# Kernel tuning notes

Hardware: AMD Instinct MI355X
Metric: run time of the kernel (lower is better)

The kernel has to match this reference:

```python
import jax, jax.numpy as jnp
import numpy as np
from jax import lax

THRESH = 0.6      # pnet score threshold (threshold[0])
IOU_THR = 0.5     # per-scale nms threshold in detect_face
K_PICKS = 128     # fixed max number of NMS picks (jit-static)
STRIDE = 2.0
CELL = 12.0
NEG = -1e30


def _conv(x, w, b):
    y = lax.conv_general_dilated(x, w, (1, 1), 'VALID',
                                 dimension_numbers=('NCHW', 'OIHW', 'NCHW'))
    return y + b[None, :, None, None]


def _prelu(x, a):
    return jnp.where(x > 0, x, a[None, :, None, None] * x)


def _maxpool2(x):
    return lax.reduce_window(x, -jnp.inf, lax.max, (1, 1, 2, 2), (1, 1, 2, 2), 'VALID')


def _nms(boxes, scores):
    # Greedy union-IoU NMS (nms_numpy math), vectorized with a fixed pick budget.
    # boxes [N,4] (shared grid), scores [N] with invalid entries already = NEG.
    x1, y1, x2, y2 = boxes[:, 0], boxes[:, 1], boxes[:, 2], boxes[:, 3]
    area = (x2 - x1 + 1.0) * (y2 - y1 + 1.0)

    def body(live, _):
        j = jnp.argmax(live)
        s = live[j]
        ok = s > NEG * 0.5
        xx1 = jnp.maximum(x1[j], x1); yy1 = jnp.maximum(y1[j], y1)
        xx2 = jnp.minimum(x2[j], x2); yy2 = jnp.minimum(y2[j], y2)
        inter = jnp.maximum(0.0, xx2 - xx1 + 1.0) * jnp.maximum(0.0, yy2 - yy1 + 1.0)
        iou = inter / (area[j] + area - inter)
        live = jnp.where(iou > IOU_THR, NEG, live).at[j].set(NEG)
        return live, (j, ok)

    _, (idx, ok) = lax.scan(body, scores, None, length=K_PICKS)
    return idx, ok


def setup_inputs():
    key = jax.random.key(0)
    ks = jax.random.split(key, 16)
    B, H, W = 16, 384, 512
    f = lambda k, shp, s=0.1: jax.random.normal(k, shp, jnp.float32) * s
    return {
        'im_data': jax.random.uniform(ks[0], (B, 3, H, W), jnp.float32) * 255.0,
        'c1_w': f(ks[1], (10, 3, 3, 3)), 'c1_b': f(ks[2], (10,)),
        'p1': jnp.full((10,), 0.25, jnp.float32),
        'c2_w': f(ks[3], (16, 10, 3, 3)), 'c2_b': f(ks[4], (16,)),
        'p2': jnp.full((16,), 0.25, jnp.float32),
        'c3_w': f(ks[5], (32, 16, 3, 3)), 'c3_b': f(ks[6], (32,)),
        'p3': jnp.full((32,), 0.25, jnp.float32),
        'c41_w': f(ks[7], (2, 32, 1, 1)), 'c41_b': f(ks[8], (2,)),
        'c42_w': f(ks[9], (4, 32, 1, 1)), 'c42_b': f(ks[10], (4,)),
    }


def reference(im_data, c1_w, c1_b, p1, c2_w, c2_b, p2, c3_w, c3_b, p3,
              c41_w, c41_b, c42_w, c42_b):
    # --- PNet conv trunk (detect_face normalization + MTCNN PNet) ---
    x = (im_data - 127.5) * 0.0078125
    h = _prelu(_conv(x, c1_w, c1_b), p1)
    h = _maxpool2(h)                                   # 2x2 s2 (dims even -> ceil==floor)
    h = _prelu(_conv(h, c2_w, c2_b), p2)
    h = _prelu(_conv(h, c3_w, c3_b), p3)
    probs = jax.nn.softmax(_conv(h, c41_w, c41_b), axis=1)[:, 1]   # [B,Hp,Wp]
    reg = _conv(h, c42_w, c42_b)                                   # [B,4,Hp,Wp]

    # --- generateBoundingBox (dense, masked instead of nonzero; scale=1) ---
    B, Hp, Wp = probs.shape
    yy, xx = jnp.meshgrid(jnp.arange(Hp, dtype=jnp.float32),
                          jnp.arange(Wp, dtype=jnp.float32), indexing='ij')
    boxes4 = jnp.stack([jnp.floor(STRIDE * xx + 1.0).ravel(),
                        jnp.floor(STRIDE * yy + 1.0).ravel(),
                        jnp.floor(STRIDE * xx + CELL).ravel(),
                        jnp.floor(STRIDE * yy + CELL).ravel()], axis=1)  # [N,4]
    scores = probs.reshape(B, -1)                                   # [B,N]
    regf = reg.reshape(B, 4, -1).transpose(0, 2, 1)                 # [B,N,4]
    masked = jnp.where(scores >= THRESH, scores, NEG)

    # --- per-image greedy NMS (batched_nms: images independent) ---
    idx, ok = jax.vmap(_nms, in_axes=(None, 0))(boxes4, masked)     # [B,K]
    pb = boxes4[idx]                                                # [B,K,4]
    ps = jnp.take_along_axis(scores, idx, axis=1)                   # [B,K]
    pr = jnp.take_along_axis(regf, idx[..., None], axis=1)          # [B,K,4]

    w = pb[..., 2] - pb[..., 0]
    hh = pb[..., 3] - pb[..., 1]
    q1 = pb[..., 0] + pr[..., 0] * w
    q2 = pb[..., 1] + pr[..., 1] * hh
    q3 = pb[..., 2] + pr[..., 2] * w
    q4 = pb[..., 3] + pr[..., 3] * hh
    rw = q3 - q1
    rh = q4 - q2
    l = jnp.maximum(rw, rh)
    nx1 = q1 + rw * 0.5 - l * 0.5
    ny1 = q2 + rh * 0.5 - l * 0.5
    out = jnp.stack([nx1, ny1, nx1 + l, ny1 + l, ps], axis=-1)      # [B,K,5]
    return out * ok[..., None].astype(out.dtype)
```

## Files before the change

kernel.cpp:

```cpp
#include <hip/hip_runtime.h>
#include <math.h>

#define BATCH 16
#define IH 384
#define IW 512
#define C1 10
#define P1H 191
#define P1W 255
#define P1S 256
#define C2 16
#define H2 189
#define W2 253
#define C3 32
#define H3 187
#define W3 251
#define N3 (H3*W3)
#define KP 128
#define CAP 7680
#define NEGV (-1e30f)

typedef _Float16 f16x8 __attribute__((ext_vector_type(8)));
typedef _Float16 f16x4 __attribute__((ext_vector_type(4)));
typedef float    f32x16 __attribute__((ext_vector_type(16)));

#define PXT 66
#define PXT2 68
#define NSUB 2

#define T1R 34
#define T1C 68
__global__ __launch_bounds__(256, 1) void k_conv1pool(
        const float* __restrict__ im, const float* __restrict__ w,
        const float* __restrict__ bia, const float* __restrict__ slope,
        float* __restrict__ outp,
        const float* __restrict__ w3, const float* __restrict__ w2,
        _Float16* __restrict__ wbuf, _Float16* __restrict__ wbuf2) {
    __shared__ float T[3 * T1R * T1C];

    int tx = threadIdx.x, ty = threadIdx.y;
    int tid = ty * 16 + tx;
    int bx = blockIdx.x, by = blockIdx.y, bb = blockIdx.z;

    if (bx == 0 && by == 0 && bb == 0) {
        for (int e = tid; e < 4608; e += 256) {
            int oc = e / 144;
            int rem = e - oc * 144;
            int ic = rem / 9;
            int tap = rem - ic * 9;
            float v = w3[e];
            _Float16 h = (_Float16)v;
            _Float16 l = (_Float16)(v - (float)h);
            int d = ((tap * 2 + (ic >> 3)) * 32 + oc) * 8 + (ic & 7);
            wbuf[d] = h;
            wbuf[4608 + d] = l;
        }
        for (int e = tid; e < 4608; e += 256) {
            int tap = e / 512;
            int rem = e - tap * 512;
            int half = rem >> 8;
            int oc = (rem >> 3) & 31;
            int j = e & 7;
            int ic = half * 8 + j;
            float v = 0.f;
            if (oc < 16 && ic < 10) v = w2[(oc * 10 + ic) * 9 + tap];
            _Float16 h = (_Float16)v;
            wbuf2[e] = h;
            wbuf2[4608 + e] = (_Float16)(v - (float)h);
        }
    }

    const size_t ibase = (size_t)bb * 3 * IH * IW;
    for (int g = tid; g < 3 * T1R * 33; g += 256) {
        int ch = g / (T1R * 33);
        int rem = g - ch * (T1R * 33);
        int r = rem / 33;
        int c2 = rem - r * 33;
        int yg = 32 * by + r;
        int xg = 64 * bx + 2 * c2;
        float2 v = make_float2(0.f, 0.f);
        if (yg < IH && xg < IW)
            v = *(const float2*)(im + ibase + ((size_t)ch * IH + yg) * IW + xg);
        float2 o;
        o.x = (v.x - 127.5f) * 0.0078125f;
        o.y = (v.y - 127.5f) * 0.0078125f;
        *(float2*)&T[(ch * T1R + r) * T1C + 2 * c2] = o;
    }
    __syncthreads();

    int Y  = by * 16 + ty;
    int X0 = bx * 32 + 2 * tx;
    if (Y >= P1H) return;

    float win[3][4][6];
    #pragma unroll
    for (int ch = 0; ch < 3; ++ch)
        #pragma unroll
        for (int r = 0; r < 4; ++r) {
            const float* p = &T[(ch * T1R + 2 * ty + r) * T1C + 4 * tx];
            float4 a = *(const float4*)p;
            float2 b = *(const float2*)(p + 4);
            win[ch][r][0] = a.x; win[ch][r][1] = a.y;
            win[ch][r][2] = a.z; win[ch][r][3] = a.w;
            win[ch][r][4] = b.x; win[ch][r][5] = b.y;
        }
    #pragma unroll
    for (int ch = 0; ch < 3; ++ch)
        #pragma unroll
        for (int r = 0; r < 4; ++r)
            #pragma unroll
            for (int c = 0; c < 6; ++c)
                asm volatile("" : "+v"(win[ch][r][c]));

    bool px1ok = (X0 + 1 < P1W);
    for (int oc = 0; oc < C1; ++oc) {
        const float* wo = w + oc * 27;
        float bv = bia[oc], sv = slope[oc];
        float c0 = bv, c1 = bv, c2 = bv, c3 = bv;
        float c4 = bv, c5 = bv, c6 = bv, c7 = bv;
        #pragma unroll
        for (int ch = 0; ch < 3; ++ch)
            #pragma unroll
            for (int ky = 0; ky < 3; ++ky)
                #pragma unroll
                for (int kx = 0; kx < 3; ++kx) {
                    float wv = wo[(ch * 3 + ky) * 3 + kx];
                    c0 += win[ch][0 + ky][0 + kx] * wv;
                    c1 += win[ch][0 + ky][1 + kx] * wv;
                    c2 += win[ch][0 + ky][2 + kx] * wv;
                    c3 += win[ch][0 + ky][3 + kx] * wv;
                    c4 += win[ch][1 + ky][0 + kx] * wv;
                    c5 += win[ch][1 + ky][1 + kx] * wv;
                    c6 += win[ch][1 + ky][2 + kx] * wv;
                    c7 += win[ch][1 + ky][3 + kx] * wv;
                }
        float m0 = fmaxf(fmaxf(c0, c1), fmaxf(c4, c5));
        float m1 = fmaxf(fmaxf(c2, c3), fmaxf(c6, c7));
        float p0 = m0 > 0.f ? m0 : sv * m0;
        float p1 = m1 > 0.f ? m1 : sv * m1;
        float* o = outp + (((size_t)bb * C1 + oc) * P1H + Y) * P1S + X0;
        if (px1ok) *(float2*)o = make_float2(p0, p1);
        else       o[0] = p0;
    }
}

__global__ __launch_bounds__(256, 2) void k_conv2mfma(
        const float* __restrict__ pool1,
        const _Float16* __restrict__ wbuf2,
        const float* __restrict__ b2, const float* __restrict__ s2,
        float* __restrict__ outp) {
    __shared__ __align__(16) _Float16 Ah[6 * 2 * PXT2 * 8];
    __shared__ __align__(16) _Float16 Al[6 * 2 * PXT2 * 8];
    __shared__ float htab[32];

    int tid = threadIdx.x;
    int bx = blockIdx.x * 64;
    int by = blockIdx.y * 4;
    int bb = blockIdx.z;

    if (tid < 32) htab[tid] = (tid < 16) ? b2[tid] : s2[tid - 16];

    {
        const float* pin = pool1 + (size_t)bb * C1 * P1H * P1S;
        for (int e = tid; e < 6 * 16 * 17; e += 256) {
            int row = e / (16 * 17);
            int rem = e - row * (16 * 17);
            int ic  = rem / 17;
            int c4  = (rem - ic * 17) * 4;
            int yg = by + row;
            int xg = bx + c4;
            float4 v = make_float4(0.f, 0.f, 0.f, 0.f);
            if (ic < C1 && yg < P1H) {
                const float* src = pin + ((size_t)ic * P1H + yg) * P1S + xg;
                if (xg + 3 < P1W) v = *(const float4*)src;
                else {
                    if (xg     < P1W) v.x = src[0];
                    if (xg + 1 < P1W) v.y = src[1];
                    if (xg + 2 < P1W) v.z = src[2];
                }
            }
            int kg = ic >> 3, j = ic & 7;
            int base = ((row * 2 + kg) * PXT2 + c4) * 8 + j;
            _Float16 h;
            h = (_Float16)v.x; Ah[base]      = h; Al[base]      = (_Float16)(v.x - (float)h);
            h = (_Float16)v.y; Ah[base + 8]  = h; Al[base + 8]  = (_Float16)(v.y - (float)h);
            h = (_Float16)v.z; Ah[base + 16] = h; Al[base + 16] = (_Float16)(v.z - (float)h);
            h = (_Float16)v.w; Ah[base + 24] = h; Al[base + 24] = (_Float16)(v.w - (float)h);
        }
    }
    __syncthreads();

    int wv = tid >> 6, lane = tid & 63;
    int col = lane & 31, half = lane >> 5;
    int y = by + wv;
    if (y >= H2) return;

    f32x16 acc[NSUB];
    #pragma unroll
    for (int s = 0; s < NSUB; ++s)
        #pragma unroll
        for (int i = 0; i < 16; ++i) acc[s][i] = 0.f;

    const _Float16* wg = wbuf2 + (half * 32 + col) * 8;

    #pragma unroll 1
    for (int ky = 0; ky < 3; ++ky) {
        const _Float16* arh = Ah + ((wv + ky) * 2 + half) * (PXT2 * 8);
        const _Float16* arl = Al + ((wv + ky) * 2 + half) * (PXT2 * 8);
        #pragma unroll
        for (int kx = 0; kx < 3; ++kx) {
            int tap = ky * 3 + kx;
            f16x8 wh = *(const f16x8*)(wg + tap * 512);
            f16x8 wl = *(const f16x8*)(wg + 4608 + tap * 512);
            #pragma unroll
            for (int s = 0; s < NSUB; ++s) {
                int p = s * 32 + col + kx;
                f16x8 bh = *(const f16x8*)(arh + p * 8);
                f16x8 bl = *(const f16x8*)(arl + p * 8);
                acc[s] = __builtin_amdgcn_mfma_f32_32x32x16_f16(wh, bh, acc[s], 0, 0, 0);
                acc[s] = __builtin_amdgcn_mfma_f32_32x32x16_f16(wl, bh, acc[s], 0, 0, 0);
                acc[s] = __builtin_amdgcn_mfma_f32_32x32x16_f16(wh, bl, acc[s], 0, 0, 0);
            }
        }
    }

    int oc0 = 4 * half, oc1 = 8 + 4 * half;
    #pragma unroll
    for (int s = 0; s < NSUB; ++s) {
        int px = bx + s * 32 + col;
        if (px < W2) {
            float q[8];
            #pragma unroll
            for (int r = 0; r < 8; ++r) {
                int oc = (r < 4) ? (oc0 + r) : (oc1 + r - 4);
                float v = acc[s][r] + htab[oc];
                float sl = htab[16 + oc];
                q[r] = v > 0.f ? v : sl * v;
            }
            float* o = outp + (((size_t)bb * H2 + y) * W2 + px) * C2;
            *(float4*)(o + oc0) = make_float4(q[0], q[1], q[2], q[3]);
            *(float4*)(o + oc1) = make_float4(q[4], q[5], q[6], q[7]);
        }
    }
}

__global__ __launch_bounds__(256, 2) void k_conv3mfma(
        const float* __restrict__ act,
        const _Float16* __restrict__ wbuf,
        const float* __restrict__ b3, const float* __restrict__ s3,
        const float* __restrict__ w41, const float* __restrict__ b41,
        const float* __restrict__ w42, const float* __restrict__ b42,
        float* __restrict__ scores, float4* __restrict__ regf) {
    __shared__ __align__(16) _Float16 Ah[6 * 2 * PXT * 8];
    __shared__ __align__(16) _Float16 Al[6 * 2 * PXT * 8];
    __shared__ __align__(16) float    htab[32 * 8];

    int tid = threadIdx.x;
    int bx = blockIdx.x * (NSUB * 32);
    int by = blockIdx.y * 4;
    int bb = blockIdx.z;

    {
        int oc = tid >> 3, f = tid & 7;
        float v;
        if      (f == 0) v = b3[oc];
        else if (f == 1) v = s3[oc];
        else if (f == 2) v = w41[oc];
        else if (f == 3) v = w41[32 + oc];
        else             v = w42[(f - 4) * 32 + oc];
        htab[tid] = v;
    }
    {
        const float* actb = act + (size_t)bb * H2 * W2 * C2;
        for (int e = tid; e < 6 * PXT * 4; e += 256) {
            int ic4 = e & 3;
            int t = e >> 2;
            int px = t % PXT;
            int row = t / PXT;
            int yg = by + row, xg = bx + px;
            float4 v = make_float4(0.f, 0.f, 0.f, 0.f);
            if (yg < H2 && xg < W2)
                v = *(const float4*)(actb + ((size_t)yg * W2 + xg) * C2 + ic4 * 4);
            float xs0 = v.x, xs1 = v.y, xs2 = v.z, xs3 = v.w;
            f16x4 hv, lv;
            _Float16 h;
            h = (_Float16)xs0; hv[0] = h; lv[0] = (_Float16)(xs0 - (float)h);
            h = (_Float16)xs1; hv[1] = h; lv[1] = (_Float16)(xs1 - (float)h);
            h = (_Float16)xs2; hv[2] = h; lv[2] = (_Float16)(xs2 - (float)h);
            h = (_Float16)xs3; hv[3] = h; lv[3] = (_Float16)(xs3 - (float)h);
            int kg = ic4 >> 1, h4 = ic4 & 1;
            int gr = (row * 2 + kg) * PXT + px;
            *(f16x4*)(Ah + gr * 8 + h4 * 4) = hv;
            *(f16x4*)(Al + gr * 8 + h4 * 4) = lv;
        }
    }
    __syncthreads();

    int wv = tid >> 6, lane = tid & 63;
    int col = lane & 31, half = lane >> 5;
    int y = by + wv;
    if (y >= H3) return;

    f32x16 acc[NSUB];
    #pragma unroll
    for (int s = 0; s < NSUB; ++s)
        #pragma unroll
        for (int i = 0; i < 16; ++i) acc[s][i] = 0.f;

    const _Float16* wg = wbuf + (half * 32 + col) * 8;

    #pragma unroll 1
    for (int ky = 0; ky < 3; ++ky) {
        const _Float16* arh = Ah + ((wv + ky) * 2 + half) * (PXT * 8);
        const _Float16* arl = Al + ((wv + ky) * 2 + half) * (PXT * 8);
        #pragma unroll
        for (int kx = 0; kx < 3; ++kx) {
            int tap = ky * 3 + kx;
            f16x8 wh = *(const f16x8*)(wg + tap * 512);
            f16x8 wl = *(const f16x8*)(wg + 4608 + tap * 512);
            #pragma unroll
            for (int s = 0; s < NSUB; ++s) {
                int p = s * 32 + col + kx;
                f16x8 bh = *(const f16x8*)(arh + p * 8);
                f16x8 bl = *(const f16x8*)(arl + p * 8);
                acc[s] = __builtin_amdgcn_mfma_f32_32x32x16_f16(wh, bh, acc[s], 0, 0, 0);
                acc[s] = __builtin_amdgcn_mfma_f32_32x32x16_f16(wl, bh, acc[s], 0, 0, 0);
                acc[s] = __builtin_amdgcn_mfma_f32_32x32x16_f16(wh, bl, acc[s], 0, 0, 0);
            }
        }
    }

    float L0[NSUB], L1[NSUB], R0[NSUB], R1[NSUB], R2[NSUB], R3[NSUB];
    #pragma unroll
    for (int s = 0; s < NSUB; ++s) { L0[s]=0.f; L1[s]=0.f; R0[s]=0.f; R1[s]=0.f; R2[s]=0.f; R3[s]=0.f; }

    #pragma unroll
    for (int r = 0; r < 16; ++r) {
        int oc = (r & 3) + 8 * (r >> 2) + 4 * half;
        float4 t0 = *(const float4*)&htab[oc * 8];
        float4 t1 = *(const float4*)&htab[oc * 8 + 4];
        #pragma unroll
        for (int s = 0; s < NSUB; ++s) {
            float v = acc[s][r] + t0.x;
            v = v > 0.f ? v : v * t0.y;
            L0[s] += v * t0.z; L1[s] += v * t0.w;
            R0[s] += v * t1.x; R1[s] += v * t1.y;
            R2[s] += v * t1.z; R3[s] += v * t1.w;
        }
    }

    float hb0 = b41[0], hb1 = b41[1];
    float rb0 = b42[0], rb1 = b42[1], rb2 = b42[2], rb3 = b42[3];

    #pragma unroll
    for (int s = 0; s < NSUB; ++s) {
        float l0 = L0[s] + __shfl_xor(L0[s], 32) + hb0;
        float l1 = L1[s] + __shfl_xor(L1[s], 32) + hb1;
        float r0 = R0[s] + __shfl_xor(R0[s], 32) + rb0;
        float r1 = R1[s] + __shfl_xor(R1[s], 32) + rb1;
        float r2 = R2[s] + __shfl_xor(R2[s], 32) + rb2;
        float r3 = R3[s] + __shfl_xor(R3[s], 32) + rb3;
        float m = fmaxf(l0, l1);
        float e0 = expf(l0 - m), e1 = expf(l1 - m);
        float p = e1 / (e0 + e1);
        int px = bx + s * 32 + col;
        if (half == 0 && px < W3) {
            size_t n = (size_t)bb * N3 + (size_t)y * W3 + px;
            scores[n] = (p >= 0.6f) ? p : NEGV;
            regf[n] = make_float4(r0, r1, r2, r3);
        }
    }
}

__global__ __launch_bounds__(512) void k_nms(
        const float* __restrict__ scores, const float4* __restrict__ regf,
        float* __restrict__ outp) {
    __shared__ float s_score[CAP];
    __shared__ int   s_idx[CAP];
    __shared__ float r_s[2][8];
    __shared__ int   r_i[2][8];
    __shared__ float s_picks[KP];
    __shared__ int   s_picki[KP];
    __shared__ int   s_misc[4];

    int tid = threadIdx.x;
    int bb = blockIdx.x;
    const float* sc = scores + (size_t)bb * N3;

    if (tid < 4) s_misc[tid] = 0;
    __syncthreads();

    int cnt = 0;
    for (int i = tid; i < N3; i += 512) if (sc[i] > 0.f) cnt++;
    atomicAdd(&s_misc[0], cnt);
    __syncthreads();
    int M = s_misc[0];

    int cutbin = 0;
    if (M > CAP) {
        for (int i = tid; i < 2048; i += 512) s_idx[i] = 0;
        __syncthreads();
        for (int i = tid; i < N3; i += 512) {
            float s = sc[i];
            if (s > 0.f) {
                int b = (int)((s - 0.6f) * 5120.f);
                b = b < 0 ? 0 : (b > 2047 ? 2047 : b);
                atomicAdd(&s_idx[b], 1);
            }
        }
        __syncthreads();
        if (tid == 0) {
            int accum = 0, b = 2047;
            for (; b >= 0; --b) {
                int c = s_idx[b];
                if (accum + c > CAP) break;
                accum += c;
            }
            s_misc[2] = b + 1;
        }
        __syncthreads();
        cutbin = s_misc[2];
        __syncthreads();
    }

    for (int i = tid; i < N3; i += 512) {
        float s = sc[i];
        if (s > 0.f) {
            bool keep = true;
            if (M > CAP) {
                int b = (int)((s - 0.6f) * 5120.f);
                b = b < 0 ? 0 : (b > 2047 ? 2047 : b);
                keep = (b >= cutbin);
            }
            if (keep) {
                int pos = atomicAdd(&s_misc[1], 1);
                if (pos < CAP) { s_score[pos] = s; s_idx[pos] = i; }
            }
        }
    }
    __syncthreads();
    int M2 = s_misc[1]; if (M2 > CAP) M2 = CAP;

    int np = 0;
    int   ppi = -1;
    float px1 = 0.f, py1 = 0.f, px2 = 0.f, py2 = 0.f;
    for (int pick = 0; pick < KP; ++pick) {
        float bs = -INFINITY; int bi = 0x7fffffff;
        for (int i = tid; i < M2; i += 512) {
            float s = s_score[i];
            if (ppi >= 0 && s > NEGV * 0.5f) {
                int id = s_idx[i];
                int cx = id % W3, cy = id / W3;
                float x1 = (float)(2 * cx + 1), y1 = (float)(2 * cy + 1);
                float x2 = (float)(2 * cx + 12), y2 = (float)(2 * cy + 12);
                float xx1 = fmaxf(px1, x1), yy1 = fmaxf(py1, y1);
                float xx2 = fminf(px2, x2), yy2 = fminf(py2, y2);
                float inter = fmaxf(0.f, xx2 - xx1 + 1.f) * fmaxf(0.f, yy2 - yy1 + 1.f);
                float iou = inter / (288.f - inter);
                if (iou > 0.5f) { s = NEGV; s_score[i] = NEGV; }
            }
            int id = s_idx[i];
            if (s > bs || (s == bs && id < bi)) { bs = s; bi = id; }
        }
        #pragma unroll
        for (int off = 32; off; off >>= 1) {
            float os = __shfl_down(bs, off);
            int   oi = __shfl_down(bi, off);
            if (os > bs || (os == bs && oi < bi)) { bs = os; bi = oi; }
        }
        int lane = tid & 63, wv = tid >> 6, buf = pick & 1;
        if (lane == 0) { r_s[buf][wv] = bs; r_i[buf][wv] = bi; }
        __syncthreads();
        float ps = r_s[buf][0]; int pi = r_i[buf][0];
        #pragma unroll
        for (int k = 1; k < 8; ++k) {
            float os = r_s[buf][k]; int oi = r_i[buf][k];
            if (os > ps || (os == ps && oi < pi)) { ps = os; pi = oi; }
        }
        if (ps < 0.f) break;
        if (tid == 0) { s_picks[pick] = ps; s_picki[pick] = pi; }
        np = pick + 1;

        ppi = pi;
        int pcx = pi % W3, pcy = pi / W3;
        px1 = (float)(2 * pcx + 1);  py1 = (float)(2 * pcy + 1);
        px2 = (float)(2 * pcx + 12); py2 = (float)(2 * pcy + 12);
    }
    __syncthreads();

    if (tid < KP) {
        float* o = outp + ((size_t)bb * KP + tid) * 5;
        if (tid < np) {
            int pi = s_picki[tid]; float ps = s_picks[tid];
            int cx = pi % W3, cy = pi / W3;
            float x1 = (float)(2 * cx + 1), y1 = (float)(2 * cy + 1);
            float x2 = (float)(2 * cx + 12), y2 = (float)(2 * cy + 12);
            float4 r = regf[(size_t)bb * N3 + pi];
            float wd = x2 - x1, hh = y2 - y1;
            float q1 = x1 + r.x * wd, q2 = y1 + r.y * hh;
            float q3 = x2 + r.z * wd, q4 = y2 + r.w * hh;
            float rw = q3 - q1, rh = q4 - q2;
            float L = fmaxf(rw, rh);
            float nx1 = q1 + rw * 0.5f - L * 0.5f;
            float ny1 = q2 + rh * 0.5f - L * 0.5f;
            o[0] = nx1; o[1] = ny1; o[2] = nx1 + L; o[3] = ny1 + L; o[4] = ps;
        } else {
            o[0] = 0.f; o[1] = 0.f; o[2] = 0.f; o[3] = 0.f; o[4] = 0.f;
        }
    }
}

extern "C" void kernel_launch(void* const* d_in, const int* in_sizes, int n_in,
                              void* d_out, int out_size, void* d_ws, size_t ws_size,
                              hipStream_t stream) {
    const float* im   = (const float*)d_in[0];
    const float* c1w  = (const float*)d_in[1];
    const float* c1b  = (const float*)d_in[2];
    const float* p1   = (const float*)d_in[3];
    const float* c2w  = (const float*)d_in[4];
    const float* c2b  = (const float*)d_in[5];
    const float* p2   = (const float*)d_in[6];
    const float* c3w  = (const float*)d_in[7];
    const float* c3b  = (const float*)d_in[8];
    const float* p3   = (const float*)d_in[9];
    const float* c41w = (const float*)d_in[10];
    const float* c41b = (const float*)d_in[11];
    const float* c42w = (const float*)d_in[12];
    const float* c42b = (const float*)d_in[13];

    float* ws = (float*)d_ws;
    const size_t P1FLOATS = (size_t)BATCH * C1 * P1H * P1S;
    float*  pool1   = ws;
    float*  conv2b  = ws + P1FLOATS;
    float*  scoresb = ws;
    float4* regfb   = (float4*)(ws + (size_t)BATCH * N3);
    _Float16* wbuf  = (_Float16*)d_out;
    _Float16* wbuf2 = wbuf + 9216;

    k_conv1pool<<<dim3(8, 12, BATCH), dim3(16, 16), 0, stream>>>(im, c1w, c1b, p1, pool1,
                                                                 c3w, c2w, wbuf, wbuf2);
    k_conv2mfma<<<dim3(4, 48, BATCH), dim3(256), 0, stream>>>(pool1, wbuf2, c2b, p2, conv2b);
    k_conv3mfma<<<dim3(4, 47, BATCH), dim3(256), 0, stream>>>(conv2b, wbuf, c3b, p3,
                                                              c41w, c41b, c42w, c42b,
                                                              scoresb, regfb);
    k_nms<<<dim3(BATCH), dim3(512), 0, stream>>>(scoresb, regfb, (float*)d_out);
}
```

Baseline: 235.0 us.

## Rewrite conv1+pool kernel to use split-fp16 MFMA instead of scalar FMA

Replaces the scalar-FP32 conv1+maxpool kernel with an MFMA version. Inputs and weights are split into fp16 hi/lo pairs and laid out in LDS as im2col-like tiles, with kx as the reduction loop. Each wave computes two conv rows and max-pools them, using a lane shuffle for the horizontal pool step. The grid now uses smaller row tiles with more blocks. This aims to move conv1 arithmetic onto matrix cores, at the cost of three MFMAs per product for precision, extra LDS zeroing and scattered LDS writes, and wasted MFMA width (10 of 32 output channels, 9 of 16 K).

```diff
diff --git a/kernel.cpp b/kernel.cpp
--- a/kernel.cpp
+++ b/kernel.cpp
@@ -27,18 +27,18 @@
 #define PXT2 68
 #define NSUB 2
 
-#define T1R 34
-#define T1C 68
-__global__ __launch_bounds__(256, 1) void k_conv1pool(
-        const float* __restrict__ im, const float* __restrict__ w,
-        const float* __restrict__ bia, const float* __restrict__ slope,
+__global__ __launch_bounds__(256, 2) void k_conv1mfma(
+        const float* __restrict__ im, const float* __restrict__ w1,
+        const float* __restrict__ b1, const float* __restrict__ s1,
         float* __restrict__ outp,
         const float* __restrict__ w3, const float* __restrict__ w2,
         _Float16* __restrict__ wbuf, _Float16* __restrict__ wbuf2) {
-    __shared__ float T[3 * T1R * T1C];
-
-    int tx = threadIdx.x, ty = threadIdx.y;
-    int tid = ty * 16 + tx;
+    __shared__ __align__(16) _Float16 Ah[4 * 130 * 16];
+    __shared__ __align__(16) _Float16 Al[4 * 130 * 16];
+    __shared__ __align__(16) _Float16 Wlds[2 * 1536];
+    __shared__ float htab[20];
+
+    int tid = threadIdx.x;
     int bx = blockIdx.x, by = blockIdx.y, bb = blockIdx.z;
 
     if (bx == 0 && by == 0 && bb == 0) {
@@ -49,10 +49,9 @@
             int tap = rem - ic * 9;
             float v = w3[e];
             _Float16 h = (_Float16)v;
-            _Float16 l = (_Float16)(v - (float)h);
             int d = ((tap * 2 + (ic >> 3)) * 32 + oc) * 8 + (ic & 7);
             wbuf[d] = h;
-            wbuf[4608 + d] = l;
+            wbuf[4608 + d] = (_Float16)(v - (float)h);
         }
         for (int e = tid; e < 4608; e += 256) {
             int tap = e / 512;
@@ -69,77 +68,119 @@
         }
     }
 
-    const size_t ibase = (size_t)bb * 3 * IH * IW;
-    for (int g = tid; g < 3 * T1R * 33; g += 256) {
-        int ch = g / (T1R * 33);
-        int rem = g - ch * (T1R * 33);
-        int r = rem / 33;
-        int c2 = rem - r * 33;
-        int yg = 32 * by + r;
-        int xg = 64 * bx + 2 * c2;
-        float2 v = make_float2(0.f, 0.f);
-        if (yg < IH && xg < IW)
-            v = *(const float2*)(im + ibase + ((size_t)ch * IH + yg) * IW + xg);
-        float2 o;
-        o.x = (v.x - 127.5f) * 0.0078125f;
-        o.y = (v.y - 127.5f) * 0.0078125f;
-        *(float2*)&T[(ch * T1R + r) * T1C + 2 * c2] = o;
-    }
-    __syncthreads();
-
-    int Y  = by * 16 + ty;
-    int X0 = bx * 32 + 2 * tx;
-    if (Y >= P1H) return;
-
-    float win[3][4][6];
-    #pragma unroll
-    for (int ch = 0; ch < 3; ++ch)
-        #pragma unroll
-        for (int r = 0; r < 4; ++r) {
-            const float* p = &T[(ch * T1R + 2 * ty + r) * T1C + 4 * tx];
-            float4 a = *(const float4*)p;
-            float2 b = *(const float2*)(p + 4);
-            win[ch][r][0] = a.x; win[ch][r][1] = a.y;
-            win[ch][r][2] = a.z; win[ch][r][3] = a.w;
-            win[ch][r][4] = b.x; win[ch][r][5] = b.y;
-        }
-    #pragma unroll
-    for (int ch = 0; ch < 3; ++ch)
-        #pragma unroll
-        for (int r = 0; r < 4; ++r)
+    {
+        float4 z = make_float4(0.f, 0.f, 0.f, 0.f);
+        for (int e = tid; e < 1040; e += 256) {
+            ((float4*)Ah)[e] = z;
+            ((float4*)Al)[e] = z;
+        }
+    }
+    __syncthreads();
+
+    for (int e = tid; e < 1536; e += 256) {
+        int kx = e / 512;
+        int rem = e & 511;
+        int half = rem >> 8;
+        int oc = (rem >> 3) & 31;
+        int j = e & 7;
+        int k = half * 8 + j;
+        float v = 0.f;
+        if (oc < C1 && k < 9) {
+            int ch = k / 3, ky = k - ch * 3;
+            v = w1[oc * 27 + ch * 9 + ky * 3 + kx];
+        }
+        _Float16 h = (_Float16)v;
+        Wlds[e] = h;
+        Wlds[1536 + e] = (_Float16)(v - (float)h);
+    }
+    if (tid < C1) { htab[tid] = b1[tid]; htab[10 + tid] = s1[tid]; }
+
+    {
+        const size_t ibase = (size_t)bb * 3 * IH * IW;
+        int R0 = 4 * by, X0 = 128 * bx;
+        for (int g = tid; g < 6 * 3 * 65; g += 256) {
+            int r = g / 195;
+            int rem = g - r * 195;
+            int ch = rem / 65;
+            int c2 = rem - ch * 65;
+            int yg = R0 + r;
+            int xg = X0 + 2 * c2;
+            float2 v = make_float2(0.f, 0.f);
+            if (yg < IH && xg < IW)
+                v = *(const float2*)(im + ibase + ((size_t)ch * IH + yg) * IW + xg);
+            float a0 = (v.x - 127.5f) * 0.0078125f;
+            float a1 = (v.y - 127.5f) * 0.0078125f;
+            _Float16 h0 = (_Float16)a0, l0 = (_Float16)(a0 - (float)h0);
+            _Float16 h1 = (_Float16)a1, l1 = (_Float16)(a1 - (float)h1);
+            int px = 2 * c2;
             #pragma unroll
-            for (int c = 0; c < 6; ++c)
-                asm volatile("" : "+v"(win[ch][r][c]));
-
-    bool px1ok = (X0 + 1 < P1W);
-    for (int oc = 0; oc < C1; ++oc) {
-        const float* wo = w + oc * 27;
-        float bv = bia[oc], sv = slope[oc];
-        float c0 = bv, c1 = bv, c2 = bv, c3 = bv;
-        float c4 = bv, c5 = bv, c6 = bv, c7 = bv;
-        #pragma unroll
-        for (int ch = 0; ch < 3; ++ch)
-            #pragma unroll
-            for (int ky = 0; ky < 3; ++ky)
-                #pragma unroll
-                for (int kx = 0; kx < 3; ++kx) {
-                    float wv = wo[(ch * 3 + ky) * 3 + kx];
-                    c0 += win[ch][0 + ky][0 + kx] * wv;
-                    c1 += win[ch][0 + ky][1 + kx] * wv;
-                    c2 += win[ch][0 + ky][2 + kx] * wv;
-                    c3 += win[ch][0 + ky][3 + kx] * wv;
-                    c4 += win[ch][1 + ky][0 + kx] * wv;
-                    c5 += win[ch][1 + ky][1 + kx] * wv;
-                    c6 += win[ch][1 + ky][2 + kx] * wv;
-                    c7 += win[ch][1 + ky][3 + kx] * wv;
+            for (int dy = 0; dy < 3; ++dy) {
+                int y = r - dy;
+                if (y >= 0 && y < 4) {
+                    int k = ch * 3 + dy;
+                    int i0 = (y * 130 + px) * 16 + k;
+                    Ah[i0] = h0;      Al[i0] = l0;
+                    Ah[i0 + 16] = h1; Al[i0 + 16] = l1;
                 }
-        float m0 = fmaxf(fmaxf(c0, c1), fmaxf(c4, c5));
-        float m1 = fmaxf(fmaxf(c2, c3), fmaxf(c6, c7));
-        float p0 = m0 > 0.f ? m0 : sv * m0;
-        float p1 = m1 > 0.f ? m1 : sv * m1;
-        float* o = outp + (((size_t)bb * C1 + oc) * P1H + Y) * P1S + X0;
-        if (px1ok) *(float2*)o = make_float2(p0, p1);
-        else       o[0] = p0;
+            }
+        }
+    }
+    __syncthreads();
+
+    int wv = tid >> 6, lane = tid & 63;
+    int col = lane & 31, half = lane >> 5;
+    int pr = wv >> 1, cw = wv & 1;
+    int PY = 2 * by + pr;
+    if (PY >= P1H) return;
+    int y0 = 2 * pr, y1 = y0 + 1;
+
+    const _Float16* WH = Wlds;
+    const _Float16* WL = Wlds + 1536;
+
+    #pragma unroll
+    for (int s = 0; s < 2; ++s) {
+        int pxs = cw * 64 + s * 32;
+        f32x16 accA, accB;
+        #pragma unroll
+        for (int i = 0; i < 16; ++i) { accA[i] = 0.f; accB[i] = 0.f; }
+
+        #pragma unroll
+        for (int kx = 0; kx < 3; ++kx) {
+            f16x8 wh = *(const f16x8*)(WH + ((kx * 2 + half) * 32 + col) * 8);
+            f16x8 wl = *(const f16x8*)(WL + ((kx * 2 + half) * 32 + col) * 8);
+            int p = pxs + col + kx;
+            int i0 = (y0 * 130 + p) * 16 + half * 8;
+            int i1 = (y1 * 130 + p) * 16 + half * 8;
+            f16x8 ah0 = *(const f16x8*)(Ah + i0);
+            f16x8 al0 = *(const f16x8*)(Al + i0);
+            f16x8 ah1 = *(const f16x8*)(Ah + i1);
+            f16x8 al1 = *(const f16x8*)(Al + i1);
+            accA = __builtin_amdgcn_mfma_f32_32x32x16_f16(wh, ah0, accA, 0, 0, 0);
+            accA = __builtin_amdgcn_mfma_f32_32x32x16_f16(wl, ah0, accA, 0, 0, 0);
+            accA = __builtin_amdgcn_mfma_f32_32x32x16_f16(wh, al0, accA, 0, 0, 0);
+            accB = __builtin_amdgcn_mfma_f32_32x32x16_f16(wh, ah1, accB, 0, 0, 0);
+            accB = __builtin_amdgcn_mfma_f32_32x32x16_f16(wl, ah1, accB, 0, 0, 0);
+            accB = __builtin_amdgcn_mfma_f32_32x32x16_f16(wh, al1, accB, 0, 0, 0);
+        }
+
+        #pragma unroll
+        for (int r = 0; r < 16; ++r) {
+            int oc = (r & 3) + 8 * (r >> 2) + 4 * half;
+            if (oc < C1) {
+                float m = fmaxf(accA[r], accB[r]);
+                float o = __shfl_xor(m, 1);
+                m = fmaxf(m, o);
+                if (!(col & 1)) {
+                    int X = (128 * bx + pxs + col) >> 1;
+                    if (X < P1W) {
+                        float v = m + htab[oc];
+                        float sl = htab[10 + oc];
+                        v = v > 0.f ? v : sl * v;
+                        outp[(((size_t)bb * C1 + oc) * P1H + PY) * P1S + X] = v;
+                    }
+                }
+            }
+        }
     }
 }
 
@@ -536,8 +577,8 @@
     _Float16* wbuf  = (_Float16*)d_out;
     _Float16* wbuf2 = wbuf + 9216;
 
-    k_conv1pool<<<dim3(8, 12, BATCH), dim3(16, 16), 0, stream>>>(im, c1w, c1b, p1, pool1,
-                                                                 c3w, c2w, wbuf, wbuf2);
+    k_conv1mfma<<<dim3(4, 96, BATCH), dim3(256), 0, stream>>>(im, c1w, c1b, p1, pool1,
+                                                              c3w, c2w, wbuf, wbuf2);
     k_conv2mfma<<<dim3(4, 48, BATCH), dim3(256), 0, stream>>>(pool1, wbuf2, c2b, p2, conv2b);
     k_conv3mfma<<<dim3(4, 47, BATCH), dim3(256), 0, stream>>>(conv2b, wbuf, c3b, p3,
                                                               c41w, c41b, c42w, c42b,
```

Result: slower. 259.0 us (+10.2%).
